# Kernel tuning notes

Measured on AMD Instinct MI355X. Metric: run time of the kernel, lower is better.

Reference implementation:

```python
import jax, jax.numpy as jnp
import numpy as np

N_MEMORY, N_LOOPS, N_LATENT = 1067, 8, 128
N_CONTEXT = 64
MAX_FEAT = N_LOOPS * N_CONTEXT * N_LATENT  # 65536
BLOCK = 2048


def setup_inputs() -> dict:
    key = jax.random.key(0)
    ks = jax.random.split(key, 10)
    return {
        "memory": jax.random.normal(ks[0], (N_MEMORY, N_LOOPS, N_LATENT), jnp.float32),
        "z_in": jax.random.normal(ks[1], (N_LATENT,), jnp.float32),
        # scale weights so the F=65536 matvec output stays O(1)
        "weights": jax.random.normal(ks[2], (N_LOOPS, MAX_FEAT, N_LATENT), jnp.float32) * 0.005,
        "center": jax.random.normal(ks[3], (N_LOOPS, MAX_FEAT), jnp.float32),
        "bias": jax.random.normal(ks[4], (N_LOOPS, N_LATENT), jnp.float32),
        "z_min": jax.random.normal(ks[5], (N_LOOPS, N_LATENT), jnp.float32) - 2.0,
        "z_max": jax.random.normal(ks[6], (N_LOOPS, N_LATENT), jnp.float32) + 2.0,
        "limit_margin": jax.random.uniform(ks[7], (N_LATENT,), jnp.float32),
        "mask": jax.random.uniform(ks[8], (2, N_LOOPS), jnp.float32),
        "y_audio": jax.random.normal(ks[9], (N_LOOPS, 1, BLOCK), jnp.float32),
        "record_index": 500,
        "active_loop": 3,       # 1-indexed, as in LivingLooper.forward
        "latency_correct": 2,
        "context": N_CONTEXT,
    }


def _target_process_inv(z):
    # torch.where(z>1, 2*z**0.5 - 1, where(z<-1, 1 - 2*(-z)**0.5, z)); safe sqrt for jax where
    hi = 2.0 * jnp.sqrt(jnp.maximum(z, 1.0)) - 1.0
    lo = 1.0 - 2.0 * jnp.sqrt(jnp.maximum(-z, 1.0))
    return jnp.where(z > 1.0, hi, jnp.where(z < -1.0, lo, z))


def reference(memory, z_in, weights, center, bias, z_min, z_max,
              limit_margin, mask, y_audio, record_index, active_loop,
              latency_correct, context):
    n_memory, n_loops, n_latent = memory.shape
    i_act = active_loop - 1

    # --- ring-buffer record of new latent for active loop at dt = lc..0 ---
    rows = (record_index - np.arange(latency_correct + 1)) % n_memory
    mem1 = memory.at[rows, i_act].set(z_in)

    # --- get_frames(context, skip=1): context frames ending at record_index-1 ---
    widx = (record_index - 1 - context + 1 + np.arange(context)) % n_memory
    window = mem1[widx]                       # [ctx, n_loops, n_latent]
    flat = window.reshape(-1)                 # [F], F = ctx*n_loops*n_latent

    # --- per-loop Loop.eval: feat_process -> matvec -> inv -> clamp ---
    x = jnp.tanh((flat[None, :] - center) * 0.5)          # [L, F]
    z = jnp.einsum('lf,lfd->ld', x, weights) + bias       # [L, D]
    z = _target_process_inv(z)
    z = jnp.clip(z, z_min - limit_margin[None, :], z_max + limit_margin[None, :])

    # --- scatter eval results at record_index for all loops except active ---
    keep = (jnp.arange(n_loops) == i_act)[:, None]
    mem2 = mem1.at[record_index].set(jnp.where(keep, mem1[record_index], z))

    zs = mem2[record_index]                   # [L, D] == get_frames(1)

    # --- masked crossfade on decoded audio ---
    fade = jnp.linspace(0.0, 1.0, y_audio.shape[2])
    m = mask[1][:, None, None] * fade + mask[0][:, None, None] * (1.0 - fade)
    y = y_audio * m                           # [L, 1, block]
    return (y, zs, mem2)
```

## Files before the change

### kernel.cpp

```cpp
#include <hip/hip_runtime.h>


__global__ __launch_bounds__(256) void ll_matvec_kernel(
    const float* __restrict__ memory, const float* __restrict__ z_in,
    const float* __restrict__ weights, const float* __restrict__ center,
    const int* __restrict__ rec_p, const int* __restrict__ act_p,
    const int* __restrict__ lc_p, const int* __restrict__ ctx_p,
    float* __restrict__ zacc,
    int L, int D, int F, int n_memory, int blocksPerLoop)
{
    __shared__ float x_lds[256];
    __shared__ float ps[8 * 128];

    const int bid = blockIdx.x;
    const int l = bid / blocksPerLoop;
    const int chunk = bid - l * blocksPerLoop;
    const int f0 = chunk * 256;
    const int tid = threadIdx.x;

    const int rec = *rec_p;
    const int i_act = *act_p - 1;
    const int lc = *lc_p;
    const int ctx = *ctx_p;
    const int LD = L * D;

    {
        const int f = f0 + tid;
        const int c = f / LD;
        const int rem = f - c * LD;
        const int ll = rem / D;
        const int dd = rem - ll * D;
        int row = rec - ctx + c;
        row %= n_memory; if (row < 0) row += n_memory;
        int diff = rec - row; if (diff < 0) diff += n_memory;
        float v = (ll == i_act && diff <= lc)
                      ? z_in[dd]
                      : memory[(size_t)row * LD + rem];
        const float cen = center[(size_t)l * F + f];
        x_lds[tid] = tanhf((v - cen) * 0.5f);
    }
    __syncthreads();

    const int g = tid >> 5;
    const int t = tid & 31;
    const int d4 = t * 4;
    const float4* __restrict__ W =
        (const float4*)(weights + ((size_t)l * F + f0) * D);
    float4 acc = make_float4(0.f, 0.f, 0.f, 0.f);
    #pragma unroll 4
    for (int i = 0; i < 32; ++i) {
        const int r = i * 8 + g;
        const float xv = x_lds[r];
        const float4 w = W[(size_t)r * 32 + t];
        acc.x += xv * w.x; acc.y += xv * w.y;
        acc.z += xv * w.z; acc.w += xv * w.w;
    }
    ps[g * 128 + d4 + 0] = acc.x;
    ps[g * 128 + d4 + 1] = acc.y;
    ps[g * 128 + d4 + 2] = acc.z;
    ps[g * 128 + d4 + 3] = acc.w;
    __syncthreads();

    if (tid < 128) {
        float s = 0.f;
        #pragma unroll
        for (int gg = 0; gg < 8; ++gg) s += ps[gg * 128 + tid];
        atomicAdd(&zacc[l * D + tid], s);
    }
}

__global__ __launch_bounds__(256) void ll_misc_kernel(
    const float* __restrict__ memory, const float* __restrict__ z_in,
    const float* __restrict__ mask, const float* __restrict__ y_audio,
    const int* __restrict__ rec_p, const int* __restrict__ act_p,
    const int* __restrict__ lc_p,
    float* __restrict__ out_y, float* __restrict__ out_mem2,
    int L, int D, int n_memory, int BLK)
{
    const int idx = blockIdx.x * blockDim.x + threadIdx.x;
    const int LD = L * D;
    const int Ncopy = n_memory * LD;
    if (idx < Ncopy) {
        const int rec = *rec_p;
        const int row = idx / LD;
        if (row == rec) return;
        const int rem = idx - row * LD;
        const int ll = rem / D;
        const int dd = rem - ll * D;
        int diff = rec - row; if (diff < 0) diff += n_memory;
        float v;
        if (ll == (*act_p - 1) && diff <= *lc_p) v = z_in[dd];
        else                                     v = memory[idx];
        out_mem2[idx] = v;
    } else if (idx < Ncopy + L * BLK) {
        const int j = idx - Ncopy;
        const int l = j / BLK;
        const int k = j - l * BLK;
        const float fade = (float)k / (float)(BLK - 1);
        const float m = mask[L + l] * fade + mask[l] * (1.f - fade);
        out_y[j] = y_audio[j] * m;
    }
}

__global__ __launch_bounds__(256) void ll_finalize_kernel(
    const float* __restrict__ zacc, const float* __restrict__ bias,
    const float* __restrict__ z_min, const float* __restrict__ z_max,
    const float* __restrict__ limit_margin, const float* __restrict__ z_in,
    const int* __restrict__ rec_p, const int* __restrict__ act_p,
    float* __restrict__ out_zs, float* __restrict__ out_mem2,
    int L, int D)
{
    const int tid = blockIdx.x * blockDim.x + threadIdx.x;
    if (tid >= L * D) return;
    const int l = tid / D;
    const int d = tid - l * D;

    float z = zacc[tid] + bias[tid];
    const float hi = 2.f * sqrtf(fmaxf(z, 1.f)) - 1.f;
    const float lo = 1.f - 2.f * sqrtf(fmaxf(-z, 1.f));
    z = (z > 1.f) ? hi : ((z < -1.f) ? lo : z);
    const float zl = z_min[tid] - limit_margin[d];
    const float zh = z_max[tid] + limit_margin[d];
    z = fminf(fmaxf(z, zl), zh);

    const float out = (l == (*act_p - 1)) ? z_in[d] : z;
    out_zs[tid] = out;
    out_mem2[(size_t)(*rec_p) * (L * D) + tid] = out;
}

extern "C" void kernel_launch(void* const* d_in, const int* in_sizes, int n_in,
                              void* d_out, int out_size, void* d_ws, size_t ws_size,
                              hipStream_t stream) {
    const float* memory       = (const float*)d_in[0];
    const float* z_in         = (const float*)d_in[1];
    const float* weights      = (const float*)d_in[2];
    const float* center       = (const float*)d_in[3];
    const float* bias         = (const float*)d_in[4];
    const float* z_min        = (const float*)d_in[5];
    const float* z_max        = (const float*)d_in[6];
    const float* limit_margin = (const float*)d_in[7];
    const float* mask         = (const float*)d_in[8];
    const float* y_audio      = (const float*)d_in[9];
    const int*   rec_p        = (const int*)d_in[10];
    const int*   act_p        = (const int*)d_in[11];
    const int*   lc_p         = (const int*)d_in[12];
    const int*   ctx_p        = (const int*)d_in[13];

    const int D        = in_sizes[1];
    const int L        = in_sizes[4] / D;
    const int LD       = L * D;
    const int n_memory = in_sizes[0] / LD;
    const int F        = in_sizes[3] / L;
    const int BLK      = in_sizes[9] / L;

    float* out_y    = (float*)d_out;
    float* out_zs   = out_y + (size_t)L * BLK;
    float* out_mem2 = out_zs + LD;

    float* zacc = (float*)d_ws;
    hipMemsetAsync(zacc, 0, (size_t)LD * sizeof(float), stream);

    const int blocksPerLoop = F / 256;
    ll_matvec_kernel<<<L * blocksPerLoop, 256, 0, stream>>>(
        memory, z_in, weights, center, rec_p, act_p, lc_p, ctx_p,
        zacc, L, D, F, n_memory, blocksPerLoop);

    const int total = n_memory * LD + L * BLK;
    ll_misc_kernel<<<(total + 255) / 256, 256, 0, stream>>>(
        memory, z_in, mask, y_audio, rec_p, act_p, lc_p,
        out_y, out_mem2, L, D, n_memory, BLK);

    ll_finalize_kernel<<<(LD + 255) / 256, 256, 0, stream>>>(
        zacc, bias, z_min, z_max, limit_margin, z_in,
        rec_p, act_p, out_zs, out_mem2, L, D);
}
```

Before: 58.37 us.

## Fuse matvec with memory copy and replace atomics with per-block partials

Merges the memory-copy/audio-crossfade kernel into the matvec kernel through a grid-stride loop, and removes the memset. Instead of atomically accumulating into a zeroed buffer, each block writes its partial sums and the finalize kernel reduces them. Weight loads and output stores use nontemporal hints, and the unroll factor rises to 8. This saves two launches and the atomic contention, at the cost of a serial reduction over 256 partials per output in finalize.

```diff
diff --git a/kernel.cpp b/kernel.cpp
--- a/kernel.cpp
+++ b/kernel.cpp
@@ -1,13 +1,17 @@
 #include <hip/hip_runtime.h>
 
+typedef float v4f __attribute__((ext_vector_type(4)));
 
-__global__ __launch_bounds__(256) void ll_matvec_kernel(
+
+__global__ __launch_bounds__(256) void ll_main_kernel(
     const float* __restrict__ memory, const float* __restrict__ z_in,
     const float* __restrict__ weights, const float* __restrict__ center,
+    const float* __restrict__ mask, const float* __restrict__ y_audio,
     const int* __restrict__ rec_p, const int* __restrict__ act_p,
     const int* __restrict__ lc_p, const int* __restrict__ ctx_p,
-    float* __restrict__ zacc,
-    int L, int D, int F, int n_memory, int blocksPerLoop)
+    float* __restrict__ partials, float* __restrict__ out_y,
+    float* __restrict__ out_mem2,
+    int L, int D, int F, int n_memory, int blocksPerLoop, int BLK)
 {
     __shared__ float x_lds[256];
     __shared__ float ps[8 * 128];
@@ -43,79 +47,69 @@
 
     const int g = tid >> 5;
     const int t = tid & 31;
-    const int d4 = t * 4;
-    const float4* __restrict__ W =
-        (const float4*)(weights + ((size_t)l * F + f0) * D);
-    float4 acc = make_float4(0.f, 0.f, 0.f, 0.f);
-    #pragma unroll 4
+    const v4f* __restrict__ W = (const v4f*)(weights + ((size_t)l * F + f0) * D);
+    v4f acc = (v4f)0.f;
+    #pragma unroll 8
     for (int i = 0; i < 32; ++i) {
         const int r = i * 8 + g;
         const float xv = x_lds[r];
-        const float4 w = W[(size_t)r * 32 + t];
-        acc.x += xv * w.x; acc.y += xv * w.y;
-        acc.z += xv * w.z; acc.w += xv * w.w;
+        const v4f w = __builtin_nontemporal_load(&W[(size_t)r * 32 + t]);
+        acc += xv * w;
     }
-    ps[g * 128 + d4 + 0] = acc.x;
-    ps[g * 128 + d4 + 1] = acc.y;
-    ps[g * 128 + d4 + 2] = acc.z;
-    ps[g * 128 + d4 + 3] = acc.w;
+    ((v4f*)&ps[g * 128])[t] = acc;
     __syncthreads();
 
     if (tid < 128) {
         float s = 0.f;
         #pragma unroll
         for (int gg = 0; gg < 8; ++gg) s += ps[gg * 128 + tid];
-        atomicAdd(&zacc[l * D + tid], s);
+        partials[(size_t)bid * 128 + tid] = s;
     }
-}
 
-__global__ __launch_bounds__(256) void ll_misc_kernel(
-    const float* __restrict__ memory, const float* __restrict__ z_in,
-    const float* __restrict__ mask, const float* __restrict__ y_audio,
-    const int* __restrict__ rec_p, const int* __restrict__ act_p,
-    const int* __restrict__ lc_p,
-    float* __restrict__ out_y, float* __restrict__ out_mem2,
-    int L, int D, int n_memory, int BLK)
-{
-    const int idx = blockIdx.x * blockDim.x + threadIdx.x;
-    const int LD = L * D;
+    const int gsize = gridDim.x * 256;
     const int Ncopy = n_memory * LD;
-    if (idx < Ncopy) {
-        const int rec = *rec_p;
-        const int row = idx / LD;
-        if (row == rec) return;
-        const int rem = idx - row * LD;
-        const int ll = rem / D;
-        const int dd = rem - ll * D;
-        int diff = rec - row; if (diff < 0) diff += n_memory;
-        float v;
-        if (ll == (*act_p - 1) && diff <= *lc_p) v = z_in[dd];
-        else                                     v = memory[idx];
-        out_mem2[idx] = v;
-    } else if (idx < Ncopy + L * BLK) {
-        const int j = idx - Ncopy;
-        const int l = j / BLK;
-        const int k = j - l * BLK;
-        const float fade = (float)k / (float)(BLK - 1);
-        const float m = mask[L + l] * fade + mask[l] * (1.f - fade);
-        out_y[j] = y_audio[j] * m;
+    const int total = Ncopy + L * BLK;
+    for (int idx = bid * 256 + tid; idx < total; idx += gsize) {
+        if (idx < Ncopy) {
+            const int row = idx / LD;
+            if (row == rec) continue;
+            const int rem = idx - row * LD;
+            const int ll = rem / D;
+            const int dd = rem - ll * D;
+            int diff = rec - row; if (diff < 0) diff += n_memory;
+            const float v = (ll == i_act && diff <= lc) ? z_in[dd] : memory[idx];
+            __builtin_nontemporal_store(v, &out_mem2[idx]);
+        } else {
+            const int j = idx - Ncopy;
+            const int li = j / BLK;
+            const int k = j - li * BLK;
+            const float fade = (float)k / (float)(BLK - 1);
+            const float m = mask[L + li] * fade + mask[li] * (1.f - fade);
+            out_y[j] = y_audio[j] * m;
+        }
     }
 }
 
 __global__ __launch_bounds__(256) void ll_finalize_kernel(
-    const float* __restrict__ zacc, const float* __restrict__ bias,
+    const float* __restrict__ partials, const float* __restrict__ bias,
     const float* __restrict__ z_min, const float* __restrict__ z_max,
     const float* __restrict__ limit_margin, const float* __restrict__ z_in,
     const int* __restrict__ rec_p, const int* __restrict__ act_p,
     float* __restrict__ out_zs, float* __restrict__ out_mem2,
-    int L, int D)
+    int L, int D, int blocksPerLoop)
 {
     const int tid = blockIdx.x * blockDim.x + threadIdx.x;
     if (tid >= L * D) return;
     const int l = tid / D;
     const int d = tid - l * D;
 
-    float z = zacc[tid] + bias[tid];
+    float s = 0.f;
+    const float* __restrict__ p = partials + (size_t)l * blocksPerLoop * D + d;
+    #pragma unroll 8
+    for (int c = 0; c < blocksPerLoop; ++c)
+        s += p[(size_t)c * D];
+
+    float z = s + bias[tid];
     const float hi = 2.f * sqrtf(fmaxf(z, 1.f)) - 1.f;
     const float lo = 1.f - 2.f * sqrtf(fmaxf(-z, 1.f));
     z = (z > 1.f) ? hi : ((z < -1.f) ? lo : z);
@@ -157,20 +151,16 @@
     float* out_zs   = out_y + (size_t)L * BLK;
     float* out_mem2 = out_zs + LD;
 
-    float* zacc = (float*)d_ws;
-    hipMemsetAsync(zacc, 0, (size_t)LD * sizeof(float), stream);
+    float* partials = (float*)d_ws;
 
     const int blocksPerLoop = F / 256;
-    ll_matvec_kernel<<<L * blocksPerLoop, 256, 0, stream>>>(
-        memory, z_in, weights, center, rec_p, act_p, lc_p, ctx_p,
-        zacc, L, D, F, n_memory, blocksPerLoop);
-
-    const int total = n_memory * LD + L * BLK;
-    ll_misc_kernel<<<(total + 255) / 256, 256, 0, stream>>>(
-        memory, z_in, mask, y_audio, rec_p, act_p, lc_p,
-        out_y, out_mem2, L, D, n_memory, BLK);
+    ll_main_kernel<<<L * blocksPerLoop, 256, 0, stream>>>(
+        memory, z_in, weights, center, mask, y_audio,
+        rec_p, act_p, lc_p, ctx_p,
+        partials, out_y, out_mem2,
+        L, D, F, n_memory, blocksPerLoop, BLK);
 
     ll_finalize_kernel<<<(LD + 255) / 256, 256, 0, stream>>>(
-        zacc, bias, z_min, z_max, limit_margin, z_in,
-        rec_p, act_p, out_zs, out_mem2, L, D);
+        partials, bias, z_min, z_max, limit_margin, z_in,
+        rec_p, act_p, out_zs, out_mem2, L, D, blocksPerLoop);
 }
```

Result: no change. 59.53 us (+2.0%).
